# Kernel tuning notes

Measured on AMD Instinct MI355X. Metric: run time of the kernel, lower is better.

The kernel has to match this reference:

```python
import jax, jax.numpy as jnp
import numpy as np

EPS = 1e-06
FOCUSING_FACTOR = 3


def setup_inputs() -> dict:
    key = jax.random.key(0)
    k1, k2, k3, k4, k5 = jax.random.split(key, 5)
    N, L, H, D = 8, 4096, 8, 64
    return {
        "queries": jax.random.normal(k1, (N, L, H, D), dtype=jnp.float32),
        "keys": jax.random.normal(k2, (N, L, H, D), dtype=jnp.float32),
        "values": jax.random.normal(k3, (N, L, H, D), dtype=jnp.float32),
        "scale_param": jnp.zeros((1, 1, 1, D), dtype=jnp.float32),
        "dwc_w": jax.random.normal(k4, (D, 1, 5, 5), dtype=jnp.float32) * 0.1,
        "dwc_b": jax.random.normal(k5, (D,), dtype=jnp.float32) * 0.1,
        "height": 64,
    }


def reference(queries, keys, values, scale_param, dwc_w, dwc_b, height):
    N, L, H, D = values.shape
    width = L // height

    scale = jax.nn.softplus(scale_param)  # [1,1,1,D]
    q = (jax.nn.relu(queries) + 1e-06) / scale
    k = (jax.nn.relu(keys) + 1e-06) / scale

    q_norm = jnp.linalg.norm(q, axis=-1, keepdims=True)
    k_norm = jnp.linalg.norm(k, axis=-1, keepdims=True)
    q = q ** FOCUSING_FACTOR
    k = k ** FOCUSING_FACTOR
    q = q / jnp.linalg.norm(q, axis=-1, keepdims=True) * q_norm
    k = k / jnp.linalg.norm(k, axis=-1, keepdims=True) * k_norm

    # linear attention: kv summary [N,H,D,D], normalizer z [N,L,H]
    kv = jnp.einsum("nshd,nshv->nhdv", k, values)
    z = 1.0 / (jnp.einsum("nlhd,nhd->nlh", q, k.sum(axis=1)) + EPS)
    o = jnp.einsum("nlhd,nhdv,nlh->nlhv", q, kv, z)

    # depthwise 5x5 conv on values: 'n (h w) heads d -> (n heads) d h w'
    vf = values.reshape(N, height, width, H, D)
    vf = vf.transpose(0, 3, 4, 1, 2).reshape(N * H, D, height, width)
    vf = jax.lax.conv_general_dilated(
        vf, dwc_w,
        window_strides=(1, 1), padding=((2, 2), (2, 2)),
        dimension_numbers=("NCHW", "OIHW", "NCHW"),
        feature_group_count=D,
    ) + dwc_b[None, :, None, None]
    vf = vf.reshape(N, H, D, height, width).transpose(0, 3, 4, 1, 2)
    vf = vf.reshape(N, L, H, D)

    return o + vf
```

## Files before the change

### kernel.cpp

```cpp
#include <hip/hip_runtime.h>

typedef __attribute__((ext_vector_type(8))) short short8;
typedef __attribute__((ext_vector_type(4))) float f32x4;

#define LSEQ   4096
#define NHEAD  8
#define DCH    64
#define HEIGHT 64
#define WIDTH  64

static __device__ __forceinline__ float bfu2f(unsigned short u) {
  return __uint_as_float(((unsigned int)u) << 16);
}
static __device__ __forceinline__ unsigned short f2bfu(float f) {
  unsigned int b = __float_as_uint(f);
  b += 0x7FFFu + ((b >> 16) & 1u);
  return (unsigned short)(b >> 16);
}
static __device__ __forceinline__ float ldf(const void* p, int i, int isbf) {
  return isbf ? bfu2f(((const unsigned short*)p)[i]) : ((const float*)p)[i];
}
static __device__ __forceinline__ float softplus_inv(float sp) {
  float s = (sp > 20.f) ? sp : log1pf(expf(sp));
  return 1.f / s;
}
static __device__ __forceinline__ void unpack2(unsigned int u, float& lo, float& hi) {
  lo = __uint_as_float(u << 16);
  hi = __uint_as_float(u & 0xFFFF0000u);
}
static __device__ __forceinline__ void load8(const void* p, int gi, int isbf, float o[8]) {
  if (isbf) {
    uint4 u = *(const uint4*)((const unsigned short*)p + gi);
    unpack2(u.x, o[0], o[1]); unpack2(u.y, o[2], o[3]);
    unpack2(u.z, o[4], o[5]); unpack2(u.w, o[6], o[7]);
  } else {
    const float4* f4 = (const float4*)((const float*)p + gi);
    float4 a = f4[0], b = f4[1];
    o[0]=a.x; o[1]=a.y; o[2]=a.z; o[3]=a.w;
    o[4]=b.x; o[5]=b.y; o[6]=b.z; o[7]=b.w;
  }
}
static __device__ __forceinline__ void row_reduce2(float& a, float& b) {
  #pragma unroll
  for (int m = 1; m < 8; m <<= 1) { a += __shfl_xor(a, m, 64); b += __shfl_xor(b, m, 64); }
}
static __device__ __forceinline__ float row_reduce1(float a) {
  #pragma unroll
  for (int m = 1; m < 8; m <<= 1) a += __shfl_xor(a, m, 64);
  return a;
}

__global__ void detect_kernel(const unsigned int* __restrict__ q, int* __restrict__ flag) {
  int lane = threadIdx.x & 63;
  int hits = 0;
  #pragma unroll
  for (int i = 0; i < 4; ++i) {
    unsigned int lo = q[lane * 4 + i] & 0xFFFFu;
    unsigned int e  = (lo >> 7) & 0xFFu;
    if (lo == 0u || (e >= 110u && e <= 140u)) hits++;
  }
  #pragma unroll
  for (int m = 1; m < 64; m <<= 1) hits += __shfl_xor(hits, m, 64);
  if (lane == 0) *flag = (hits > 128) ? 1 : 0;
}

__global__ __launch_bounds__(256) void kv_kernel(
    const void* __restrict__ keys, const void* __restrict__ values,
    const void* __restrict__ scale_param,
    float* __restrict__ kv_p, float* __restrict__ ksum_g,
    const int* __restrict__ flagp, int chunks, int rows)
{
  __shared__ __align__(16) unsigned short kfT[64 * 40];
  __shared__ __align__(16) unsigned short vvT[64 * 40];
  __shared__ float red[256];

  const int isbf = *flagp;
  const int b = blockIdx.x;
  const int chunk = b % chunks;
  const int nh = b / chunks;
  const int h = nh & 7, n = nh >> 3;
  const int t = threadIdx.x, lane = t & 63, wid = t >> 6;
  const int quad = lane >> 4, m16 = lane & 15;
  const int r = lane >> 3, c = lane & 7, d0 = c * 8;
  const int s_local = wid * 8 + r;
  const int sp = s_local ^ ((c & 3) << 3);

  float inv_s[8];
  #pragma unroll
  for (int i = 0; i < 8; ++i) inv_s[i] = softplus_inv(ldf(scale_param, d0 + i, isbf));

  f32x4 acc[4];
  #pragma unroll
  for (int mt = 0; mt < 4; ++mt) acc[mt] = (f32x4){0.f, 0.f, 0.f, 0.f};
  float ksum_acc[8];
  #pragma unroll
  for (int i = 0; i < 8; ++i) ksum_acc[i] = 0.f;

  const int nsub = rows >> 5;
  for (int sub = 0; sub < nsub; ++sub) {
    const int s = chunk * rows + sub * 32 + s_local;
    const int gi = ((n * LSEQ + s) * NHEAD + h) * DCH + d0;

    float kraw[8];
    load8(keys, gi, isbf, kraw);
    float xv[8], yv[8], s2 = 0.f, s6 = 0.f;
    #pragma unroll
    for (int i = 0; i < 8; ++i) {
      xv[i] = (fmaxf(kraw[i], 0.f) + 1e-6f) * inv_s[i];
      s2 += xv[i] * xv[i];
    }
    #pragma unroll
    for (int i = 0; i < 8; ++i) {
      yv[i] = xv[i] * xv[i] * xv[i];
      s6 += yv[i] * yv[i];
    }
    row_reduce2(s2, s6);
    const float coef = sqrtf(s2 / s6);
    #pragma unroll
    for (int i = 0; i < 8; ++i) {
      float f = yv[i] * coef;
      ksum_acc[i] += f;
      kfT[(d0 + i) * 40 + sp] = f2bfu(f);
    }
    if (isbf) {
      uint4 u = *(const uint4*)((const unsigned short*)values + gi);
      unsigned short vs[8];
      *(uint4*)vs = u;
      #pragma unroll
      for (int i = 0; i < 8; ++i) vvT[(d0 + i) * 40 + sp] = vs[i];
    } else {
      float vraw[8];
      load8(values, gi, 0, vraw);
      #pragma unroll
      for (int i = 0; i < 8; ++i) vvT[(d0 + i) * 40 + sp] = f2bfu(vraw[i]);
    }
    __syncthreads();

    const int v = wid * 16 + m16;
    short8 bfr = *(const short8*)&vvT[v * 40 + (quad ^ ((v >> 3) & 3)) * 8];
    #pragma unroll
    for (int mt = 0; mt < 4; ++mt) {
      int d = mt * 16 + m16;
      short8 afr = *(const short8*)&kfT[d * 40 + (quad ^ ((d >> 3) & 3)) * 8];
      acc[mt] = __builtin_amdgcn_mfma_f32_16x16x32_bf16(afr, bfr, acc[mt], 0, 0, 0);
    }
    __syncthreads();
  }

  float* dst = kv_p + ((size_t)chunk * 64 + nh) * 4096;
  #pragma unroll
  for (int mt = 0; mt < 4; ++mt)
    #pragma unroll
    for (int rr = 0; rr < 4; ++rr) {
      int d = mt * 16 + quad * 4 + rr;
      dst[d * 64 + wid * 16 + m16] = acc[mt][rr];
    }

  #pragma unroll
  for (int i = 0; i < 8; ++i) {
    #pragma unroll
    for (int m = 8; m < 64; m <<= 1) ksum_acc[i] += __shfl_xor(ksum_acc[i], m, 64);
  }
  if (r == 0) {
    #pragma unroll
    for (int i = 0; i < 8; ++i) red[wid * 64 + d0 + i] = ksum_acc[i];
  }
  __syncthreads();
  if (t < 64) {
    float tot = red[t] + red[64 + t] + red[128 + t] + red[192 + t];
    atomicAdd(&ksum_g[nh * 64 + t], tot);
  }
}

__global__ __launch_bounds__(256) void reduce_kernel(
    const float* __restrict__ kv_p, unsigned short* __restrict__ kvb, int chunks)
{
  int cidx = blockIdx.x * 256 + threadIdx.x;
  int nh = cidx >> 12;
  int dv = cidx & 4095;
  int d = dv >> 6, v = dv & 63;
  float s = 0.f;
  for (int ch = 0; ch < chunks; ++ch)
    s += kv_p[((size_t)ch * 64 + nh) * 4096 + dv];
  kvb[(nh * 64 + v) * 64 + d] = f2bfu(s);
}

__global__ __launch_bounds__(256) void attn_kernel(
    const void* __restrict__ queries, const unsigned short* __restrict__ kvb,
    const float* __restrict__ ksum_g, const void* __restrict__ scale_param,
    void* __restrict__ out, const int* __restrict__ flagp)
{
  __shared__ __align__(16) unsigned short qf[64 * 72];

  const int isbf = *flagp;
  const int b = blockIdx.x;
  const int y = b & 63;
  const int nh = b >> 6;
  const int h = nh & 7, n = nh >> 3;
  const int t = threadIdx.x, lane = t & 63, wid = t >> 6;
  const int quad = lane >> 4, m16 = lane & 15;
  const int r = lane >> 3, c = lane & 7, d0 = c * 8;

  float inv_s[8];
  #pragma unroll
  for (int i = 0; i < 8; ++i) inv_s[i] = softplus_inv(ldf(scale_param, d0 + i, isbf));
  float ks[8];
  {
    float4 k0 = *(const float4*)&ksum_g[nh * 64 + d0];
    float4 k1 = *(const float4*)&ksum_g[nh * 64 + d0 + 4];
    ks[0]=k0.x; ks[1]=k0.y; ks[2]=k0.z; ks[3]=k0.w;
    ks[4]=k1.x; ks[5]=k1.y; ks[6]=k1.z; ks[7]=k1.w;
  }

  const unsigned short* kvrow = kvb + (nh * 64 + wid * 16 + m16) * 64;
  short8 bfr0 = *(const short8*)&kvrow[quad * 8];
  short8 bfr1 = *(const short8*)&kvrow[32 + quad * 8];

  #pragma unroll
  for (int batch = 0; batch < 2; ++batch) {
    int x = wid * 16 + batch * 8 + r;
    int gi = ((n * LSEQ + y * 64 + x) * NHEAD + h) * DCH + d0;
    float qraw[8];
    load8(queries, gi, isbf, qraw);
    float xv[8], yv[8], s2 = 0.f, s6 = 0.f;
    #pragma unroll
    for (int i = 0; i < 8; ++i) {
      xv[i] = (fmaxf(qraw[i], 0.f) + 1e-6f) * inv_s[i];
      s2 += xv[i] * xv[i];
    }
    #pragma unroll
    for (int i = 0; i < 8; ++i) {
      yv[i] = xv[i] * xv[i] * xv[i];
      s6 += yv[i] * yv[i];
    }
    row_reduce2(s2, s6);
    const float coef = sqrtf(s2 / s6);
    float f[8], dot = 0.f;
    #pragma unroll
    for (int i = 0; i < 8; ++i) { f[i] = yv[i] * coef; dot += f[i] * ks[i]; }
    dot = row_reduce1(dot);
    const float z = 1.f / (dot + 1e-6f);
    uint4 pk;
    pk.x = (unsigned int)f2bfu(f[0] * z) | ((unsigned int)f2bfu(f[1] * z) << 16);
    pk.y = (unsigned int)f2bfu(f[2] * z) | ((unsigned int)f2bfu(f[3] * z) << 16);
    pk.z = (unsigned int)f2bfu(f[4] * z) | ((unsigned int)f2bfu(f[5] * z) << 16);
    pk.w = (unsigned int)f2bfu(f[6] * z) | ((unsigned int)f2bfu(f[7] * z) << 16);
    *(uint4*)&qf[x * 72 + d0] = pk;
  }
  __syncthreads();

  const size_t obase = (((size_t)n * LSEQ + y * 64) * NHEAD + h) * DCH;
  #pragma unroll
  for (int mt = 0; mt < 4; ++mt) {
    f32x4 acc = (f32x4){0.f, 0.f, 0.f, 0.f};
    short8 a0 = *(const short8*)&qf[(mt * 16 + m16) * 72 + quad * 8];
    short8 a1 = *(const short8*)&qf[(mt * 16 + m16) * 72 + 32 + quad * 8];
    acc = __builtin_amdgcn_mfma_f32_16x16x32_bf16(a0, bfr0, acc, 0, 0, 0);
    acc = __builtin_amdgcn_mfma_f32_16x16x32_bf16(a1, bfr1, acc, 0, 0, 0);
    #pragma unroll
    for (int rr = 0; rr < 4; ++rr) {
      int x = mt * 16 + quad * 4 + rr;
      int v = wid * 16 + m16;
      size_t oi = obase + (size_t)x * (NHEAD * DCH) + v;
      if (isbf) ((unsigned short*)out)[oi] = f2bfu(acc[rr]);
      else      ((float*)out)[oi] = acc[rr];
    }
  }
}

__global__ __launch_bounds__(256) void conv_kernel(
    const void* __restrict__ values, const void* __restrict__ dwc_w,
    const void* __restrict__ dwc_b, void* __restrict__ out,
    const int* __restrict__ flagp)
{
  __shared__ __align__(16) unsigned short vs[8 * 64 * 32];
  __shared__ float wl[25 * 32];
  __shared__ float bl[32];

  const int isbf = *flagp;
  const int b = blockIdx.x;
  const int slab = b & 15;
  const int half = (b >> 4) & 1;
  const int nh = b >> 5;
  const int h = nh & 7, n = nh >> 3;
  const int y0 = slab * 4;
  const int t = threadIdx.x;

  for (int i = t; i < 800; i += 256) {
    int dloc = i / 25, tap = i - dloc * 25;
    wl[tap * 32 + dloc] = ldf(dwc_w, half * 800 + i, isbf);
  }
  if (t < 32) bl[t] = ldf(dwc_b, half * 32 + t, isbf);

  for (int it = t; it < 8 * 64 * 4; it += 256) {
    int j = it & 3;
    int xx = (it >> 2) & 63;
    int rr = it >> 8;
    int yy = y0 - 2 + rr;
    int swz = j ^ (xx & 3) ^ ((xx >> 2) & 3);
    unsigned short* dst = &vs[((rr * 64 + xx) * 32) + swz * 8];
    if (yy >= 0 && yy < HEIGHT) {
      int gi = ((n * LSEQ + yy * 64 + xx) * NHEAD + h) * DCH + half * 32 + j * 8;
      if (isbf) {
        *(uint4*)dst = *(const uint4*)((const unsigned short*)values + gi);
      } else {
        const float4* s4 = (const float4*)((const float*)values + gi);
        float4 f0 = s4[0], f1 = s4[1];
        dst[0] = f2bfu(f0.x); dst[1] = f2bfu(f0.y);
        dst[2] = f2bfu(f0.z); dst[3] = f2bfu(f0.w);
        dst[4] = f2bfu(f1.x); dst[5] = f2bfu(f1.y);
        dst[6] = f2bfu(f1.z); dst[7] = f2bfu(f1.w);
      }
    } else {
      uint4 z; z.x = z.y = z.z = z.w = 0u;
      *(uint4*)dst = z;
    }
  }
  __syncthreads();

  const int xx = t & 63, jb = t >> 6;
  float a[4][8];
  float bias8[8];
  {
    float4 b0 = *(const float4*)&bl[jb * 8];
    float4 b1 = *(const float4*)&bl[jb * 8 + 4];
    bias8[0]=b0.x; bias8[1]=b0.y; bias8[2]=b0.z; bias8[3]=b0.w;
    bias8[4]=b1.x; bias8[5]=b1.y; bias8[6]=b1.z; bias8[7]=b1.w;
  }
  #pragma unroll
  for (int rr = 0; rr < 4; ++rr)
    #pragma unroll
    for (int cc = 0; cc < 8; ++cc) a[rr][cc] = bias8[cc];

  for (int ky = 0; ky < 5; ++ky) {
    #pragma unroll
    for (int kx = 0; kx < 5; ++kx) {
      int xs = xx + kx - 2;
      if ((unsigned)xs < (unsigned)WIDTH) {
        float4 w0 = *(const float4*)&wl[(ky * 5 + kx) * 32 + jb * 8];
        float4 w1 = *(const float4*)&wl[(ky * 5 + kx) * 32 + jb * 8 + 4];
        int swz = jb ^ (xs & 3) ^ ((xs >> 2) & 3);
        #pragma unroll
        for (int rr = 0; rr < 4; ++rr) {
          uint4 pv = *(const uint4*)&vs[(((rr + ky) * 64 + xs) * 32) + swz * 8];
          float v0,v1,v2,v3,v4,v5,v6,v7;
          unpack2(pv.x, v0, v1); unpack2(pv.y, v2, v3);
          unpack2(pv.z, v4, v5); unpack2(pv.w, v6, v7);
          a[rr][0] += w0.x * v0; a[rr][1] += w0.y * v1;
          a[rr][2] += w0.z * v2; a[rr][3] += w0.w * v3;
          a[rr][4] += w1.x * v4; a[rr][5] += w1.y * v5;
          a[rr][6] += w1.z * v6; a[rr][7] += w1.w * v7;
        }
      }
    }
  }
  #pragma unroll
  for (int rr = 0; rr < 4; ++rr) {
    size_t oi = (((size_t)n * LSEQ + (y0 + rr) * 64 + xx) * NHEAD + h) * DCH
              + half * 32 + jb * 8;
    if (isbf) {
      unsigned short* op = (unsigned short*)out + oi;
      uint4 cur = *(uint4*)op;
      float c0,c1,c2,c3,c4,c5,c6,c7;
      unpack2(cur.x, c0, c1); unpack2(cur.y, c2, c3);
      unpack2(cur.z, c4, c5); unpack2(cur.w, c6, c7);
      uint4 res;
      res.x = (unsigned int)f2bfu(c0 + a[rr][0]) | ((unsigned int)f2bfu(c1 + a[rr][1]) << 16);
      res.y = (unsigned int)f2bfu(c2 + a[rr][2]) | ((unsigned int)f2bfu(c3 + a[rr][3]) << 16);
      res.z = (unsigned int)f2bfu(c4 + a[rr][4]) | ((unsigned int)f2bfu(c5 + a[rr][5]) << 16);
      res.w = (unsigned int)f2bfu(c6 + a[rr][6]) | ((unsigned int)f2bfu(c7 + a[rr][7]) << 16);
      *(uint4*)op = res;
    } else {
      float* op = (float*)out + oi;
      float4 o0 = *(float4*)op;
      float4 o1 = *(float4*)(op + 4);
      o0.x += a[rr][0]; o0.y += a[rr][1]; o0.z += a[rr][2]; o0.w += a[rr][3];
      o1.x += a[rr][4]; o1.y += a[rr][5]; o1.z += a[rr][6]; o1.w += a[rr][7];
      *(float4*)op = o0;
      *(float4*)(op + 4) = o1;
    }
  }
}

extern "C" void kernel_launch(void* const* d_in, const int* in_sizes, int n_in,
                              void* d_out, int out_size, void* d_ws, size_t ws_size,
                              hipStream_t stream) {
  int chunks = 16;
  while (chunks > 1) {
    size_t need = (size_t)chunks * 64 * 4096 * 4 + 64 * 4096 * 2 + 4096 * 4 + 64;
    if (need <= ws_size) break;
    chunks >>= 1;
  }
  const int rows = LSEQ / chunks;

  float* kv_p = (float*)d_ws;
  unsigned short* kvb = (unsigned short*)(kv_p + (size_t)chunks * 64 * 4096);
  float* ksum = (float*)(kvb + 64 * 4096);
  int* flag = (int*)(ksum + 4096);

  hipMemsetAsync(ksum, 0, 4096 * sizeof(float), stream);
  detect_kernel<<<1, 64, 0, stream>>>((const unsigned int*)d_in[0], flag);
  kv_kernel<<<64 * chunks, 256, 0, stream>>>(
      d_in[1], d_in[2], d_in[3], kv_p, ksum, flag, chunks, rows);
  reduce_kernel<<<1024, 256, 0, stream>>>(kv_p, kvb, chunks);
  attn_kernel<<<4096, 256, 0, stream>>>(
      d_in[0], kvb, ksum, d_in[3], d_out, flag);
  conv_kernel<<<64 * 32, 256, 0, stream>>>(
      d_in[2], d_in[4], d_in[5], d_out, flag);
}
```

Measured before the change: 322.4 us.

## Double-buffer LDS and prefetch next tiles in kv_kernel

Restructures the kv accumulation loop into a two-stage software pipeline. LDS tiles are double-buffered, and global loads for upcoming 32-row subtiles are issued into registers before the MFMA step on the current buffer. This lets global memory latency overlap with matrix math and drops one barrier per subtile. It costs extra LDS and registers, and it assumes an even number of subtiles (nsub).

```diff
diff --git a/kernel.cpp b/kernel.cpp
--- a/kernel.cpp
+++ b/kernel.cpp
@@ -70,8 +70,8 @@
     float* __restrict__ kv_p, float* __restrict__ ksum_g,
     const int* __restrict__ flagp, int chunks, int rows)
 {
-  __shared__ __align__(16) unsigned short kfT[64 * 40];
-  __shared__ __align__(16) unsigned short vvT[64 * 40];
+  __shared__ __align__(16) unsigned short kfT[2][64 * 40];
+  __shared__ __align__(16) unsigned short vvT[2][64 * 40];
   __shared__ float red[256];
 
   const int isbf = *flagp;
@@ -97,12 +97,35 @@
   for (int i = 0; i < 8; ++i) ksum_acc[i] = 0.f;
 
   const int nsub = rows >> 5;
-  for (int sub = 0; sub < nsub; ++sub) {
+  const int npair = nsub >> 1;
+
+  auto issue = [&](uint4& K0, uint4& K1, uint4& V0, uint4& V1, int sub) {
     const int s = chunk * rows + sub * 32 + s_local;
     const int gi = ((n * LSEQ + s) * NHEAD + h) * DCH + d0;
-
+    if (isbf) {
+      K0 = *(const uint4*)((const unsigned short*)keys + gi);
+      V0 = *(const uint4*)((const unsigned short*)values + gi);
+    } else {
+      const uint4* kp = (const uint4*)((const float*)keys + gi);
+      K0 = kp[0]; K1 = kp[1];
+      const uint4* vp = (const uint4*)((const float*)values + gi);
+      V0 = vp[0]; V1 = vp[1];
+    }
+  };
+  auto tofloat8 = [&](uint4 A, uint4 B, float o[8]) {
+    if (isbf) {
+      unpack2(A.x, o[0], o[1]); unpack2(A.y, o[2], o[3]);
+      unpack2(A.z, o[4], o[5]); unpack2(A.w, o[6], o[7]);
+    } else {
+      o[0]=__uint_as_float(A.x); o[1]=__uint_as_float(A.y);
+      o[2]=__uint_as_float(A.z); o[3]=__uint_as_float(A.w);
+      o[4]=__uint_as_float(B.x); o[5]=__uint_as_float(B.y);
+      o[6]=__uint_as_float(B.z); o[7]=__uint_as_float(B.w);
+    }
+  };
+  auto process = [&](uint4 K0, uint4 K1, uint4 V0, uint4 V1, int buf) {
     float kraw[8];
-    load8(keys, gi, isbf, kraw);
+    tofloat8(K0, K1, kraw);
     float xv[8], yv[8], s2 = 0.f, s6 = 0.f;
     #pragma unroll
     for (int i = 0; i < 8; ++i) {
@@ -120,30 +143,48 @@
     for (int i = 0; i < 8; ++i) {
       float f = yv[i] * coef;
       ksum_acc[i] += f;
-      kfT[(d0 + i) * 40 + sp] = f2bfu(f);
+      kfT[buf][(d0 + i) * 40 + sp] = f2bfu(f);
     }
     if (isbf) {
-      uint4 u = *(const uint4*)((const unsigned short*)values + gi);
-      unsigned short vs[8];
-      *(uint4*)vs = u;
+      unsigned short vs8[8];
+      *(uint4*)vs8 = V0;
       #pragma unroll
-      for (int i = 0; i < 8; ++i) vvT[(d0 + i) * 40 + sp] = vs[i];
+      for (int i = 0; i < 8; ++i) vvT[buf][(d0 + i) * 40 + sp] = vs8[i];
     } else {
       float vraw[8];
-      load8(values, gi, 0, vraw);
+      tofloat8(V0, V1, vraw);
       #pragma unroll
-      for (int i = 0; i < 8; ++i) vvT[(d0 + i) * 40 + sp] = f2bfu(vraw[i]);
-    }
-    __syncthreads();
-
+      for (int i = 0; i < 8; ++i) vvT[buf][(d0 + i) * 40 + sp] = f2bfu(vraw[i]);
+    }
+  };
+  auto mfma_step = [&](int buf) {
     const int v = wid * 16 + m16;
-    short8 bfr = *(const short8*)&vvT[v * 40 + (quad ^ ((v >> 3) & 3)) * 8];
+    short8 bfr = *(const short8*)&vvT[buf][v * 40 + (quad ^ ((v >> 3) & 3)) * 8];
     #pragma unroll
     for (int mt = 0; mt < 4; ++mt) {
       int d = mt * 16 + m16;
-      short8 afr = *(const short8*)&kfT[d * 40 + (quad ^ ((d >> 3) & 3)) * 8];
+      short8 afr = *(const short8*)&kfT[buf][d * 40 + (quad ^ ((d >> 3) & 3)) * 8];
       acc[mt] = __builtin_amdgcn_mfma_f32_16x16x32_bf16(afr, bfr, acc[mt], 0, 0, 0);
     }
+  };
+
+  uint4 kA0, kA1, vA0, vA1;
+  uint4 kB0, kB1, vB0, vB1;
+
+  issue(kA0, kA1, vA0, vA1, 0);
+  issue(kB0, kB1, vB0, vB1, 1);
+  process(kA0, kA1, vA0, vA1, 0);
+  __syncthreads();
+
+  for (int p = 0; p < npair; ++p) {
+    const int sub = 2 * p;
+    if (sub + 2 < nsub) issue(kA0, kA1, vA0, vA1, sub + 2);
+    mfma_step(0);
+    process(kB0, kB1, vB0, vB1, 1);
+    __syncthreads();
+    if (sub + 3 < nsub) issue(kB0, kB1, vB0, vB1, sub + 3);
+    mfma_step(1);
+    if (sub + 2 < nsub) process(kA0, kA1, vA0, vA1, 0);
     __syncthreads();
   }
 
```

Measured after the change: 333.7 us. 1.04x slower.

## Double-buffer kv LDS tiles, batch bf16 loads, remap conv threads, raise chunk count

Applied to the files above, without the earlier changes.

In kv_kernel, the bf16 path now issues four key/value row-group loads up front and ping-pongs between two LDS buffers. This lets the MFMA on one tile overlap the normalization and stores of the next, and removes one barrier per step. The depthwise conv thread mapping changes so that adjacent threads cover channel groups instead of x positions. The number of L-chunks in the kv reduction doubles to 32, which adds parallelism but gives the reduce kernel more partials to sum. The fp32 input path keeps the single-buffer loop, and the bf16 path assumes nsub is a multiple of 4.

```diff
diff --git a/kernel.cpp b/kernel.cpp
--- a/kernel.cpp
+++ b/kernel.cpp
@@ -70,8 +70,8 @@
     float* __restrict__ kv_p, float* __restrict__ ksum_g,
     const int* __restrict__ flagp, int chunks, int rows)
 {
-  __shared__ __align__(16) unsigned short kfT[64 * 40];
-  __shared__ __align__(16) unsigned short vvT[64 * 40];
+  __shared__ __align__(16) unsigned short kfT[2][64 * 40];
+  __shared__ __align__(16) unsigned short vvT[2][64 * 40];
   __shared__ float red[256];
 
   const int isbf = *flagp;
@@ -97,12 +97,8 @@
   for (int i = 0; i < 8; ++i) ksum_acc[i] = 0.f;
 
   const int nsub = rows >> 5;
-  for (int sub = 0; sub < nsub; ++sub) {
-    const int s = chunk * rows + sub * 32 + s_local;
-    const int gi = ((n * LSEQ + s) * NHEAD + h) * DCH + d0;
-
-    float kraw[8];
-    load8(keys, gi, isbf, kraw);
+
+  auto norm_k = [&](const float kraw[8], int buf) {
     float xv[8], yv[8], s2 = 0.f, s6 = 0.f;
     #pragma unroll
     for (int i = 0; i < 8; ++i) {
@@ -120,31 +116,66 @@
     for (int i = 0; i < 8; ++i) {
       float f = yv[i] * coef;
       ksum_acc[i] += f;
-      kfT[(d0 + i) * 40 + sp] = f2bfu(f);
-    }
-    if (isbf) {
-      uint4 u = *(const uint4*)((const unsigned short*)values + gi);
-      unsigned short vs[8];
-      *(uint4*)vs = u;
-      #pragma unroll
-      for (int i = 0; i < 8; ++i) vvT[(d0 + i) * 40 + sp] = vs[i];
-    } else {
+      kfT[buf][(d0 + i) * 40 + sp] = f2bfu(f);
+    }
+  };
+  auto procb = [&](uint4 K, uint4 V, int buf) {
+    float kraw[8];
+    unpack2(K.x, kraw[0], kraw[1]); unpack2(K.y, kraw[2], kraw[3]);
+    unpack2(K.z, kraw[4], kraw[5]); unpack2(K.w, kraw[6], kraw[7]);
+    norm_k(kraw, buf);
+    unsigned short vs8[8];
+    *(uint4*)vs8 = V;
+    #pragma unroll
+    for (int i = 0; i < 8; ++i) vvT[buf][(d0 + i) * 40 + sp] = vs8[i];
+  };
+  auto mfma_step = [&](int buf) {
+    const int v = wid * 16 + m16;
+    short8 bfr = *(const short8*)&vvT[buf][v * 40 + (quad ^ ((v >> 3) & 3)) * 8];
+    #pragma unroll
+    for (int mt = 0; mt < 4; ++mt) {
+      int d = mt * 16 + m16;
+      short8 afr = *(const short8*)&kfT[buf][d * 40 + (quad ^ ((d >> 3) & 3)) * 8];
+      acc[mt] = __builtin_amdgcn_mfma_f32_16x16x32_bf16(afr, bfr, acc[mt], 0, 0, 0);
+    }
+  };
+
+  if (isbf) {
+    const unsigned short* kp = (const unsigned short*)keys;
+    const unsigned short* vp = (const unsigned short*)values;
+    uint4 k0, k1, k2, k3, v0, v1, v2, v3;
+    for (int g = 0; g < nsub; g += 4) {
+      const int s = chunk * rows + g * 32 + s_local;
+      const size_t gi = ((size_t)(n * LSEQ + s) * NHEAD + h) * DCH + d0;
+      k0 = *(const uint4*)(kp + gi);
+      v0 = *(const uint4*)(vp + gi);
+      k1 = *(const uint4*)(kp + gi + 16384);
+      v1 = *(const uint4*)(vp + gi + 16384);
+      k2 = *(const uint4*)(kp + gi + 32768);
+      v2 = *(const uint4*)(vp + gi + 32768);
+      k3 = *(const uint4*)(kp + gi + 49152);
+      v3 = *(const uint4*)(vp + gi + 49152);
+      procb(k0, v0, 0); __syncthreads();
+      mfma_step(0); procb(k1, v1, 1); __syncthreads();
+      mfma_step(1); procb(k2, v2, 0); __syncthreads();
+      mfma_step(0); procb(k3, v3, 1); __syncthreads();
+      mfma_step(1);
+    }
+  } else {
+    for (int sub = 0; sub < nsub; ++sub) {
+      const int s = chunk * rows + sub * 32 + s_local;
+      const int gi = ((n * LSEQ + s) * NHEAD + h) * DCH + d0;
+      float kraw[8];
+      load8(keys, gi, 0, kraw);
+      norm_k(kraw, 0);
       float vraw[8];
       load8(values, gi, 0, vraw);
       #pragma unroll
-      for (int i = 0; i < 8; ++i) vvT[(d0 + i) * 40 + sp] = f2bfu(vraw[i]);
-    }
-    __syncthreads();
-
-    const int v = wid * 16 + m16;
-    short8 bfr = *(const short8*)&vvT[v * 40 + (quad ^ ((v >> 3) & 3)) * 8];
-    #pragma unroll
-    for (int mt = 0; mt < 4; ++mt) {
-      int d = mt * 16 + m16;
-      short8 afr = *(const short8*)&kfT[d * 40 + (quad ^ ((d >> 3) & 3)) * 8];
-      acc[mt] = __builtin_amdgcn_mfma_f32_16x16x32_bf16(afr, bfr, acc[mt], 0, 0, 0);
-    }
-    __syncthreads();
+      for (int i = 0; i < 8; ++i) vvT[0][(d0 + i) * 40 + sp] = f2bfu(vraw[i]);
+      __syncthreads();
+      mfma_step(0);
+      __syncthreads();
+    }
   }
 
   float* dst = kv_p + ((size_t)chunk * 64 + nh) * 4096;
@@ -318,7 +349,7 @@
   }
   __syncthreads();
 
-  const int xx = t & 63, jb = t >> 6;
+  const int xx = t >> 2, jb = t & 3;
   float a[4][8];
   float bias8[8];
   {
@@ -385,7 +416,7 @@
 extern "C" void kernel_launch(void* const* d_in, const int* in_sizes, int n_in,
                               void* d_out, int out_size, void* d_ws, size_t ws_size,
                               hipStream_t stream) {
-  int chunks = 16;
+  int chunks = 32;
   while (chunks > 1) {
     size_t need = (size_t)chunks * 64 * 4096 * 4 + 64 * 4096 * 2 + 4096 * 4 + 64;
     if (need <= ws_size) break;
```

After: 315.6 us. 2.1% less time.
